# Kernel optimization log

Hardware: AMD Instinct MI355X
Metric: run time of the kernel (lower is better)

Reference implementation:

```python
import jax, jax.numpy as jnp
import numpy as np

B, H, S, D = 2, 16, 2048, 128


def setup_inputs() -> dict:
    key = jax.random.key(0)
    ks = jax.random.split(key, 11)
    s = 1.0 / np.sqrt(D)
    return {
        "query": jax.random.normal(ks[0], (B, H, S, D), dtype=jnp.float32),
        "key": jax.random.normal(ks[1], (B, H, S, D), dtype=jnp.float32),
        "value": jax.random.normal(ks[2], (B, H, S, D), dtype=jnp.float32),
        "Wq": jax.random.normal(ks[3], (D, D), dtype=jnp.float32) * s,
        "bq": jnp.zeros((D,), dtype=jnp.float32),
        "Wk": jax.random.normal(ks[4], (D, D), dtype=jnp.float32) * s,
        "bk": jnp.zeros((D,), dtype=jnp.float32),
        "Wv": jax.random.normal(ks[5], (D, D), dtype=jnp.float32) * s,
        "bv": jnp.zeros((D,), dtype=jnp.float32),
        "Wo": jax.random.normal(ks[6], (D, D), dtype=jnp.float32) * s,
        "bo": jnp.zeros((D,), dtype=jnp.float32),
    }


def reference(query, key, value, Wq, bq, Wk, bk, Wv, bv, Wo, bo):
    # Linear projections (torch Linear: x @ W^T + b) on last dim of [B,H,S,D]
    q = jnp.einsum("bhsd,ed->bhse", query, Wq) + bq
    k = jnp.einsum("bhsd,ed->bhse", key, Wk) + bk
    v = jnp.einsum("bhsd,ed->bhse", value, Wv) + bv
    scale = jnp.sqrt(jnp.asarray(D, dtype=q.dtype))
    q = q / scale
    qk = jnp.einsum("bhse,bhte->bhst", q, k)  # [B,H,S,S] scores
    attn = jax.nn.softmax(qk, axis=-1)
    # dropout_p = 0.0 -> identity
    out = jnp.einsum("bhst,bhtd->bhsd", attn, v)
    out = jnp.einsum("bhsd,ed->bhse", out, Wo) + bo
    return out
```

## Files before the change

### kernel.cpp

```cpp
#include <hip/hip_runtime.h>
#include <hip/hip_bf16.h>
#include <type_traits>
#include <math.h>

typedef __bf16 bf16x8 __attribute__((ext_vector_type(8)));
typedef float floatx4 __attribute__((ext_vector_type(4)));
typedef float floatx16 __attribute__((ext_vector_type(16)));

#define S_LEN 2048
#define D_DIM 128
#define NTOK (2 * 16 * 2048)
#define KVB 64
#define NKV (S_LEN / KVB)

template <typename TIN, typename TOUT>
__device__ __forceinline__ void proj_body4(
    const TIN* __restrict__ x, const float* __restrict__ W,
    const float* __restrict__ b, TOUT* __restrict__ y, float out_scale,
    int chunk0, __bf16 (*Wl)[128]) {
  const int tid = threadIdx.x;
  const int wave = tid >> 6, lane = tid & 63;
  const int g = lane >> 4, lr = lane & 15;

  for (int it = 0; it < 16; ++it) {
    int lin = it * 1024 + tid * 4;
    float4 w4 = *reinterpret_cast<const float4*>(W + lin);
    int r = lin >> 7, c = lin & 127;
    Wl[r][c]     = (__bf16)w4.x;
    Wl[r][c + 1] = (__bf16)w4.y;
    Wl[r][c + 2] = (__bf16)w4.z;
    Wl[r][c + 3] = (__bf16)w4.w;
  }
  __syncthreads();

  float be[8];
#pragma unroll
  for (int nt = 0; nt < 8; ++nt) be[nt] = b[nt * 16 + lr];

  for (int ch = 0; ch < 4; ++ch) {
    const int rbase = (chunk0 + ch) * 64;
    const int arow = rbase + wave * 16 + lr;

    floatx4 acc[8];
#pragma unroll
    for (int i = 0; i < 8; ++i) acc[i] = floatx4{0.f, 0.f, 0.f, 0.f};

#pragma unroll
    for (int kc = 0; kc < 4; ++kc) {
      bf16x8 af;
      const TIN* xp = x + (size_t)arow * D_DIM + kc * 32 + g * 8;
      if constexpr (std::is_same<TIN, float>::value) {
        float4 f0 = *reinterpret_cast<const float4*>(xp);
        float4 f1 = *reinterpret_cast<const float4*>(xp + 4);
        af[0] = (__bf16)f0.x; af[1] = (__bf16)f0.y;
        af[2] = (__bf16)f0.z; af[3] = (__bf16)f0.w;
        af[4] = (__bf16)f1.x; af[5] = (__bf16)f1.y;
        af[6] = (__bf16)f1.z; af[7] = (__bf16)f1.w;
      } else {
        af = *reinterpret_cast<const bf16x8*>(xp);
      }
#pragma unroll
      for (int nt = 0; nt < 8; ++nt) {
        bf16x8 wf = *reinterpret_cast<const bf16x8*>(&Wl[nt * 16 + lr][kc * 32 + g * 8]);
        acc[nt] = __builtin_amdgcn_mfma_f32_16x16x32_bf16(af, wf, acc[nt], 0, 0, 0);
      }
    }

#pragma unroll
    for (int nt = 0; nt < 8; ++nt) {
      int e = nt * 16 + lr;
#pragma unroll
      for (int j = 0; j < 4; ++j) {
        int row = rbase + wave * 16 + g * 4 + j;
        float val = (acc[nt][j] + be[nt]) * out_scale;
        y[(size_t)row * D_DIM + e] = (TOUT)val;
      }
    }
  }
}

__global__ __launch_bounds__(256) void qkv_proj_kernel(
    const float* __restrict__ xq, const float* __restrict__ xk,
    const float* __restrict__ xv, const float* __restrict__ Wq,
    const float* __restrict__ Wk, const float* __restrict__ Wv,
    const float* __restrict__ bq, const float* __restrict__ bk,
    const float* __restrict__ bv, __bf16* yq, __bf16* yk, __bf16* yv,
    float qscale) {
  __shared__ alignas(16) __bf16 Wl[128][128];
  const int which = blockIdx.y;
  const float* x = which == 0 ? xq : which == 1 ? xk : xv;
  const float* W = which == 0 ? Wq : which == 1 ? Wk : Wv;
  const float* b = which == 0 ? bq : which == 1 ? bk : bv;
  __bf16* y = which == 0 ? yq : which == 1 ? yk : yv;
  float sc = which == 0 ? qscale : 1.0f;
  proj_body4<float, __bf16>(x, W, b, y, sc, blockIdx.x * 4, Wl);
}

__global__ __launch_bounds__(256) void o_proj_kernel(
    const __bf16* __restrict__ x, const float* __restrict__ W,
    const float* __restrict__ b, float* __restrict__ y) {
  __shared__ alignas(16) __bf16 Wl[128][128];
  proj_body4<__bf16, float>(x, W, b, y, 1.0f, blockIdx.x * 4, Wl);
}

__device__ __forceinline__ unsigned swz(int row, unsigned byteoff) {
  return byteoff ^ (((unsigned)(row ^ (row >> 3)) & 7u) << 4);
}

__device__ __forceinline__ unsigned pack2(float lo, float hi) {
  union { __bf16 h[2]; unsigned u; } r;
  r.h[0] = (__bf16)lo; r.h[1] = (__bf16)hi;
  return r.u;
}

__global__ __launch_bounds__(256, 2) void attn_fused_kernel(
    const __bf16* __restrict__ q, const __bf16* __restrict__ k,
    const __bf16* __restrict__ v, const float* __restrict__ Wo,
    const float* __restrict__ bo, float* __restrict__ out) {
  __shared__ alignas(16) unsigned char smem[65536];

  const int tid = threadIdx.x;
  const int wave = tid >> 6, lane = tid & 63;
  const int ql = lane & 31;
  const int h = lane >> 5;

  const int bh = blockIdx.x;
  const int qbase = blockIdx.y * 128;
  const __bf16* qp = q + (size_t)bh * S_LEN * D_DIM;
  const __bf16* kp = k + (size_t)bh * S_LEN * D_DIM;
  const __bf16* vp = v + (size_t)bh * S_LEN * D_DIM;

  const int qrow = qbase + wave * 32 + ql;
  bf16x8 qf[8];
#pragma unroll
  for (int kc = 0; kc < 8; ++kc)
    qf[kc] = *reinterpret_cast<const bf16x8*>(
        qp + (size_t)qrow * D_DIM + kc * 16 + h * 8);

  floatx16 ot[4];
#pragma unroll
  for (int d = 0; d < 4; ++d)
#pragma unroll
    for (int r = 0; r < 16; ++r) ot[d][r] = 0.f;
  float m_r = -1e30f, l_r = 0.f;

  const int cc = tid & 15;
  const int pr4 = (tid >> 4) * 4;
  const int ce = cc * 8;

  unsigned Rk[4];
#pragma unroll
  for (int x = 0; x < 4; ++x)
    Rk[x] = (unsigned)(h * 1024) +
            (((unsigned)(ql * 16)) ^ ((unsigned)h << 4) ^ ((unsigned)x << 5));
  const unsigned Rv0 = 32768u + (unsigned)(h * 2048) +
                       (((unsigned)(ql * 16)) ^ (((unsigned)(ql >> 3)) << 4));
  const unsigned Rv1 = Rv0 ^ 64u;
  const unsigned kx = ((unsigned)(cc & 7)) << 4;
  unsigned Wk_[4];
#pragma unroll
  for (int j = 0; j < 4; ++j)
    Wk_[j] = ((unsigned)(cc * 1024 + (pr4 + j) * 16)) ^ kx;
  unsigned Wv_[8];
  {
    unsigned vbase = 32768u + (unsigned)((pr4 >> 3) * 2048 + ce * 16 + (pr4 & 7) * 2);
#pragma unroll
    for (int e = 0; e < 8; ++e)
      Wv_[e] = vbase | (((unsigned)e << 4) ^ kx);
  }

  {
    const __bf16* kr = kp + (size_t)pr4 * D_DIM + ce;
    const __bf16* vr = vp + (size_t)pr4 * D_DIM + ce;
    bf16x8 kR[4];
    union { bf16x8 v8; unsigned short s[8]; } vR[4];
#pragma unroll
    for (int j = 0; j < 4; ++j) {
      kR[j] = *reinterpret_cast<const bf16x8*>(kr + j * D_DIM);
      vR[j].v8 = *reinterpret_cast<const bf16x8*>(vr + j * D_DIM);
    }
#pragma unroll
    for (int j = 0; j < 4; ++j)
      *reinterpret_cast<bf16x8*>(smem + Wk_[j]) = kR[j];
#pragma unroll
    for (int e = 0; e < 8; ++e) {
      uint2 w;
      w.x = (unsigned)vR[0].s[e] | ((unsigned)vR[1].s[e] << 16);
      w.y = (unsigned)vR[2].s[e] | ((unsigned)vR[3].s[e] << 16);
      *reinterpret_cast<uint2*>(smem + Wv_[e]) = w;
    }
  }

  const __bf16* krp = kp + ((size_t)KVB + pr4) * D_DIM + ce;
  const __bf16* vrp = vp + ((size_t)KVB + pr4) * D_DIM + ce;

#pragma unroll 2
  for (int t = 0; t < NKV; ++t) {
    const unsigned cb = (unsigned)(t & 1) * 16384u;
    const bool hn = (t + 1 < NKV);

    __syncthreads();

    bf16x8 kR[4];
    union { bf16x8 v8; unsigned short s[8]; } vR[4];
    if (hn) {
#pragma unroll
      for (int j = 0; j < 4; ++j) {
        kR[j] = *reinterpret_cast<const bf16x8*>(krp + j * D_DIM);
        vR[j].v8 = *reinterpret_cast<const bf16x8*>(vrp + j * D_DIM);
      }
      krp += (size_t)KVB * D_DIM;
      vrp += (size_t)KVB * D_DIM;
    }

    floatx16 st[2];
#pragma unroll
    for (int kvh = 0; kvh < 2; ++kvh)
#pragma unroll
      for (int r = 0; r < 16; ++r) st[kvh][r] = 0.f;
    __builtin_amdgcn_s_setprio(1);
#pragma unroll
    for (int kc = 0; kc < 8; ++kc) {
      bf16x8 kf0 = *reinterpret_cast<const bf16x8*>(
          smem + cb + Rk[kc & 3] + (unsigned)(kc * 2048));
      bf16x8 kf1 = *reinterpret_cast<const bf16x8*>(
          smem + cb + Rk[kc & 3] + (unsigned)(kc * 2048 + 512));
      st[0] = __builtin_amdgcn_mfma_f32_32x32x16_bf16(kf0, qf[kc], st[0], 0, 0, 0);
      st[1] = __builtin_amdgcn_mfma_f32_32x32x16_bf16(kf1, qf[kc], st[1], 0, 0, 0);
    }
    __builtin_amdgcn_s_setprio(0);

    if (hn) {
      const unsigned nb = cb ^ 16384u;
#pragma unroll
      for (int j = 0; j < 4; ++j)
        *reinterpret_cast<bf16x8*>(smem + nb + Wk_[j]) = kR[j];
#pragma unroll
      for (int e = 0; e < 8; ++e) {
        uint2 w;
        w.x = (unsigned)vR[0].s[e] | ((unsigned)vR[1].s[e] << 16);
        w.y = (unsigned)vR[2].s[e] | ((unsigned)vR[3].s[e] << 16);
        *reinterpret_cast<uint2*>(smem + nb + Wv_[e]) = w;
      }
    }

    float t8[8];
#pragma unroll
    for (int i = 0; i < 8; ++i)
      t8[i] = fmaxf(fmaxf(st[0][i], st[0][i + 8]), fmaxf(st[1][i], st[1][i + 8]));
    float pmax = fmaxf(fmaxf(fmaxf(t8[0], t8[4]), fmaxf(t8[1], t8[5])),
                       fmaxf(fmaxf(t8[2], t8[6]), fmaxf(t8[3], t8[7])));
    pmax = fmaxf(pmax, __shfl_xor(pmax, 32));
    if (!__all(pmax - m_r <= 8.0f)) {
      float mnew = fmaxf(m_r, pmax);
      float sc_f = __builtin_amdgcn_exp2f(m_r - mnew);
      m_r = mnew;
      l_r *= sc_f;
#pragma unroll
      for (int d = 0; d < 4; ++d)
#pragma unroll
        for (int r = 0; r < 16; ++r) ot[d][r] *= sc_f;
    }
#pragma unroll
    for (int kvh = 0; kvh < 2; ++kvh)
#pragma unroll
      for (int r = 0; r < 16; ++r)
        st[kvh][r] = __builtin_amdgcn_exp2f(st[kvh][r] - m_r);
    float s8[8];
#pragma unroll
    for (int i = 0; i < 8; ++i)
      s8[i] = (st[0][i] + st[0][i + 8]) + (st[1][i] + st[1][i + 8]);
    float psum = ((s8[0] + s8[4]) + (s8[1] + s8[5])) +
                 ((s8[2] + s8[6]) + (s8[3] + s8[7]));
    psum += __shfl_xor(psum, 32);
    l_r += psum;

#pragma unroll
    for (int ks = 0; ks < 4; ++ks) {
      const int kvh = ks >> 1;
      const int r2a = (2 * ks) & 3;
      const int r2b = r2a + 1;
      unsigned ua0 = pack2(st[kvh][r2a * 4 + 0], st[kvh][r2a * 4 + 1]);
      unsigned ua1 = pack2(st[kvh][r2a * 4 + 2], st[kvh][r2a * 4 + 3]);
      unsigned ub0 = pack2(st[kvh][r2b * 4 + 0], st[kvh][r2b * 4 + 1]);
      unsigned ub1 = pack2(st[kvh][r2b * 4 + 2], st[kvh][r2b * 4 + 3]);
      union { unsigned u[4]; bf16x8 v8; } pw;
#if __has_builtin(__builtin_amdgcn_permlane32_swap)
      {
        auto r0 = __builtin_amdgcn_permlane32_swap(ua0, ub0, false, false);
        auto r1 = __builtin_amdgcn_permlane32_swap(ua1, ub1, false, false);
        pw.u[0] = r0[0];
        pw.u[1] = r1[0];
        pw.u[2] = r0[1];
        pw.u[3] = r1[1];
      }
#else
      {
        unsigned a0x = __shfl_xor(ua0, 32), a1x = __shfl_xor(ua1, 32);
        unsigned b0x = __shfl_xor(ub0, 32), b1x = __shfl_xor(ub1, 32);
        pw.u[0] = h ? b0x : ua0;
        pw.u[1] = h ? b1x : ua1;
        pw.u[2] = h ? ub0 : a0x;
        pw.u[3] = h ? ub1 : a1x;
      }
#endif
      __builtin_amdgcn_s_setprio(1);
#pragma unroll
      for (int db = 0; db < 4; ++db) {
        const unsigned base = (db & 1) ? Rv1 : Rv0;
        bf16x8 vf = *reinterpret_cast<const bf16x8*>(
            smem + cb + base + (unsigned)(ks * 4096 + db * 512));
        ot[db] = __builtin_amdgcn_mfma_f32_32x32x16_bf16(vf, pw.v8, ot[db], 0, 0, 0);
      }
      __builtin_amdgcn_s_setprio(0);
    }
  }

  __syncthreads();

  {
    const float inv_l = 1.0f / l_r;
    const int qloc = wave * 32 + ql;
#pragma unroll
    for (int db = 0; db < 4; ++db)
#pragma unroll
      for (int r = 0; r < 16; ++r) {
        int d = db * 32 + (r & 3) + 8 * (r >> 2) + 4 * h;
        *reinterpret_cast<__bf16*>(smem + swz(qloc, qloc * 256u + d * 2u)) =
            (__bf16)(ot[db][r] * inv_l);
      }
  }
  for (int it = 0; it < 16; ++it) {
    int lin = it * 1024 + tid * 4;
    float4 w4 = *reinterpret_cast<const float4*>(Wo + lin);
    int r = lin >> 7, c = lin & 127;
    unsigned off = 32768u + swz(r, (unsigned)(r * 256 + c * 2));
    __bf16 b4[4] = {(__bf16)w4.x, (__bf16)w4.y, (__bf16)w4.z, (__bf16)w4.w};
    *reinterpret_cast<uint2*>(smem + off) = *reinterpret_cast<uint2*>(b4);
  }
  __syncthreads();

  const int g4 = lane >> 4;
  const int lr = lane & 15;
  float be[8];
#pragma unroll
  for (int nt = 0; nt < 8; ++nt) be[nt] = bo[nt * 16 + lr];

#pragma unroll
  for (int rt = 0; rt < 2; ++rt) {
    const int arow = wave * 32 + rt * 16 + lr;
    floatx4 acc[8];
#pragma unroll
    for (int i = 0; i < 8; ++i) acc[i] = floatx4{0.f, 0.f, 0.f, 0.f};
#pragma unroll
    for (int kc = 0; kc < 4; ++kc) {
      bf16x8 af = *reinterpret_cast<const bf16x8*>(
          smem + swz(arow, (unsigned)(arow * 256 + (kc * 32 + g4 * 8) * 2)));
#pragma unroll
      for (int nt = 0; nt < 8; ++nt) {
        int wrow = nt * 16 + lr;
        bf16x8 wf = *reinterpret_cast<const bf16x8*>(
            smem + 32768u + swz(wrow, (unsigned)(wrow * 256 + (kc * 32 + g4 * 8) * 2)));
        acc[nt] = __builtin_amdgcn_mfma_f32_16x16x32_bf16(af, wf, acc[nt], 0, 0, 0);
      }
    }
#pragma unroll
    for (int nt = 0; nt < 8; ++nt) {
      int e = nt * 16 + lr;
#pragma unroll
      for (int j = 0; j < 4; ++j) {
        int row = qbase + wave * 32 + rt * 16 + g4 * 4 + j;
        out[((size_t)bh * S_LEN + row) * D_DIM + e] = acc[nt][j] + be[nt];
      }
    }
  }
}

__global__ __launch_bounds__(256, 2) void attn_kernel(
    const __bf16* __restrict__ q, const __bf16* __restrict__ k,
    const __bf16* __restrict__ v, __bf16* __restrict__ o) {
  __shared__ alignas(16) unsigned char smem[65536];

  const int tid = threadIdx.x;
  const int wave = tid >> 6, lane = tid & 63;
  const int ql = lane & 31;
  const int h = lane >> 5;

  const int bh = blockIdx.x;
  const int qbase = blockIdx.y * 128;
  const __bf16* qp = q + (size_t)bh * S_LEN * D_DIM;
  const __bf16* kp = k + (size_t)bh * S_LEN * D_DIM;
  const __bf16* vp = v + (size_t)bh * S_LEN * D_DIM;
  __bf16* op = o + (size_t)bh * S_LEN * D_DIM;

  const int qrow = qbase + wave * 32 + ql;
  bf16x8 qf[8];
#pragma unroll
  for (int kc = 0; kc < 8; ++kc)
    qf[kc] = *reinterpret_cast<const bf16x8*>(
        qp + (size_t)qrow * D_DIM + kc * 16 + h * 8);

  floatx16 ot[4];
#pragma unroll
  for (int d = 0; d < 4; ++d)
#pragma unroll
    for (int r = 0; r < 16; ++r) ot[d][r] = 0.f;
  float m_r = -1e30f, l_r = 0.f;

  const int cc = tid & 15;
  const int pr4 = (tid >> 4) * 4;
  const int ce = cc * 8;

  unsigned Rk[4];
#pragma unroll
  for (int x = 0; x < 4; ++x)
    Rk[x] = (unsigned)(h * 1024) +
            (((unsigned)(ql * 16)) ^ ((unsigned)h << 4) ^ ((unsigned)x << 5));
  const unsigned Rv0 = 32768u + (unsigned)(h * 2048) +
                       (((unsigned)(ql * 16)) ^ (((unsigned)(ql >> 3)) << 4));
  const unsigned Rv1 = Rv0 ^ 64u;
  const unsigned kx = ((unsigned)(cc & 7)) << 4;
  unsigned Wk_[4];
#pragma unroll
  for (int j = 0; j < 4; ++j)
    Wk_[j] = ((unsigned)(cc * 1024 + (pr4 + j) * 16)) ^ kx;
  unsigned Wv_[8];
  {
    unsigned vbase = 32768u + (unsigned)((pr4 >> 3) * 2048 + ce * 16 + (pr4 & 7) * 2);
#pragma unroll
    for (int e = 0; e < 8; ++e)
      Wv_[e] = vbase | (((unsigned)e << 4) ^ kx);
  }

  {
    const __bf16* kr = kp + (size_t)pr4 * D_DIM + ce;
    const __bf16* vr = vp + (size_t)pr4 * D_DIM + ce;
    bf16x8 kR[4];
    union { bf16x8 v8; unsigned short s[8]; } vR[4];
#pragma unroll
    for (int j = 0; j < 4; ++j) {
      kR[j] = *reinterpret_cast<const bf16x8*>(kr + j * D_DIM);
      vR[j].v8 = *reinterpret_cast<const bf16x8*>(vr + j * D_DIM);
    }
#pragma unroll
    for (int j = 0; j < 4; ++j)
      *reinterpret_cast<bf16x8*>(smem + Wk_[j]) = kR[j];
#pragma unroll
    for (int e = 0; e < 8; ++e) {
      uint2 w;
      w.x = (unsigned)vR[0].s[e] | ((unsigned)vR[1].s[e] << 16);
      w.y = (unsigned)vR[2].s[e] | ((unsigned)vR[3].s[e] << 16);
      *reinterpret_cast<uint2*>(smem + Wv_[e]) = w;
    }
  }

  const __bf16* krp = kp + ((size_t)KVB + pr4) * D_DIM + ce;
  const __bf16* vrp = vp + ((size_t)KVB + pr4) * D_DIM + ce;

#pragma unroll 2
  for (int t = 0; t < NKV; ++t) {
    const unsigned cb = (unsigned)(t & 1) * 16384u;
    const bool hn = (t + 1 < NKV);

    __syncthreads();

    bf16x8 kR[4];
    union { bf16x8 v8; unsigned short s[8]; } vR[4];
    if (hn) {
#pragma unroll
      for (int j = 0; j < 4; ++j) {
        kR[j] = *reinterpret_cast<const bf16x8*>(krp + j * D_DIM);
        vR[j].v8 = *reinterpret_cast<const bf16x8*>(vrp + j * D_DIM);
      }
      krp += (size_t)KVB * D_DIM;
      vrp += (size_t)KVB * D_DIM;
    }

    floatx16 st[2];
#pragma unroll
    for (int kvh = 0; kvh < 2; ++kvh)
#pragma unroll
      for (int r = 0; r < 16; ++r) st[kvh][r] = 0.f;
    __builtin_amdgcn_s_setprio(1);
#pragma unroll
    for (int kc = 0; kc < 8; ++kc) {
      bf16x8 kf0 = *reinterpret_cast<const bf16x8*>(
          smem + cb + Rk[kc & 3] + (unsigned)(kc * 2048));
      bf16x8 kf1 = *reinterpret_cast<const bf16x8*>(
          smem + cb + Rk[kc & 3] + (unsigned)(kc * 2048 + 512));
      st[0] = __builtin_amdgcn_mfma_f32_32x32x16_bf16(kf0, qf[kc], st[0], 0, 0, 0);
      st[1] = __builtin_amdgcn_mfma_f32_32x32x16_bf16(kf1, qf[kc], st[1], 0, 0, 0);
    }
    __builtin_amdgcn_s_setprio(0);

    if (hn) {
      const unsigned nb = cb ^ 16384u;
#pragma unroll
      for (int j = 0; j < 4; ++j)
        *reinterpret_cast<bf16x8*>(smem + nb + Wk_[j]) = kR[j];
#pragma unroll
      for (int e = 0; e < 8; ++e) {
        uint2 w;
        w.x = (unsigned)vR[0].s[e] | ((unsigned)vR[1].s[e] << 16);
        w.y = (unsigned)vR[2].s[e] | ((unsigned)vR[3].s[e] << 16);
        *reinterpret_cast<uint2*>(smem + nb + Wv_[e]) = w;
      }
    }

    float t8[8];
#pragma unroll
    for (int i = 0; i < 8; ++i)
      t8[i] = fmaxf(fmaxf(st[0][i], st[0][i + 8]), fmaxf(st[1][i], st[1][i + 8]));
    float pmax = fmaxf(fmaxf(fmaxf(t8[0], t8[4]), fmaxf(t8[1], t8[5])),
                       fmaxf(fmaxf(t8[2], t8[6]), fmaxf(t8[3], t8[7])));
    pmax = fmaxf(pmax, __shfl_xor(pmax, 32));
    if (!__all(pmax - m_r <= 8.0f)) {
      float mnew = fmaxf(m_r, pmax);
      float sc_f = __builtin_amdgcn_exp2f(m_r - mnew);
      m_r = mnew;
      l_r *= sc_f;
#pragma unroll
      for (int d = 0; d < 4; ++d)
#pragma unroll
        for (int r = 0; r < 16; ++r) ot[d][r] *= sc_f;
    }
#pragma unroll
    for (int kvh = 0; kvh < 2; ++kvh)
#pragma unroll
      for (int r = 0; r < 16; ++r)
        st[kvh][r] = __builtin_amdgcn_exp2f(st[kvh][r] - m_r);
    float s8[8];
#pragma unroll
    for (int i = 0; i < 8; ++i)
      s8[i] = (st[0][i] + st[0][i + 8]) + (st[1][i] + st[1][i + 8]);
    float psum = ((s8[0] + s8[4]) + (s8[1] + s8[5])) +
                 ((s8[2] + s8[6]) + (s8[3] + s8[7]));
    psum += __shfl_xor(psum, 32);
    l_r += psum;

#pragma unroll
    for (int ks = 0; ks < 4; ++ks) {
      const int kvh = ks >> 1;
      const int r2a = (2 * ks) & 3;
      const int r2b = r2a + 1;
      unsigned ua0 = pack2(st[kvh][r2a * 4 + 0], st[kvh][r2a * 4 + 1]);
      unsigned ua1 = pack2(st[kvh][r2a * 4 + 2], st[kvh][r2a * 4 + 3]);
      unsigned ub0 = pack2(st[kvh][r2b * 4 + 0], st[kvh][r2b * 4 + 1]);
      unsigned ub1 = pack2(st[kvh][r2b * 4 + 2], st[kvh][r2b * 4 + 3]);
      union { unsigned u[4]; bf16x8 v8; } pw;
#if __has_builtin(__builtin_amdgcn_permlane32_swap)
      {
        auto r0 = __builtin_amdgcn_permlane32_swap(ua0, ub0, false, false);
        auto r1 = __builtin_amdgcn_permlane32_swap(ua1, ub1, false, false);
        pw.u[0] = r0[0];
        pw.u[1] = r1[0];
        pw.u[2] = r0[1];
        pw.u[3] = r1[1];
      }
#else
      {
        unsigned a0x = __shfl_xor(ua0, 32), a1x = __shfl_xor(ua1, 32);
        unsigned b0x = __shfl_xor(ub0, 32), b1x = __shfl_xor(ub1, 32);
        pw.u[0] = h ? b0x : ua0;
        pw.u[1] = h ? b1x : ua1;
        pw.u[2] = h ? ub0 : a0x;
        pw.u[3] = h ? ub1 : a1x;
      }
#endif
      __builtin_amdgcn_s_setprio(1);
#pragma unroll
      for (int db = 0; db < 4; ++db) {
        const unsigned base = (db & 1) ? Rv1 : Rv0;
        bf16x8 vf = *reinterpret_cast<const bf16x8*>(
            smem + cb + base + (unsigned)(ks * 4096 + db * 512));
        ot[db] = __builtin_amdgcn_mfma_f32_32x32x16_bf16(vf, pw.v8, ot[db], 0, 0, 0);
      }
      __builtin_amdgcn_s_setprio(0);
    }
  }

  __syncthreads();
  const float inv_l = 1.0f / l_r;
  const int qloc = wave * 32 + ql;
#pragma unroll
  for (int db = 0; db < 4; ++db)
#pragma unroll
    for (int r = 0; r < 16; ++r) {
      int d = db * 32 + (r & 3) + 8 * (r >> 2) + 4 * h;
      *reinterpret_cast<__bf16*>(smem + swz(qloc, qloc * 256u + d * 2u)) =
          (__bf16)(ot[db][r] * inv_l);
    }
  __syncthreads();
#pragma unroll
  for (int it = 0; it < 8; ++it) {
    int r = tid >> 1;
    int c = (tid & 1) * 64 + it * 8;
    bf16x8 val = *reinterpret_cast<const bf16x8*>(smem + swz(r, r * 256u + c * 2u));
    *reinterpret_cast<bf16x8*>(op + (size_t)(qbase + r) * D_DIM + c) = val;
  }
}

extern "C" void kernel_launch(void* const* d_in, const int* in_sizes, int n_in,
                              void* d_out, int out_size, void* d_ws, size_t ws_size,
                              hipStream_t stream) {
  const float* query = (const float*)d_in[0];
  const float* key_  = (const float*)d_in[1];
  const float* value = (const float*)d_in[2];
  const float* Wq = (const float*)d_in[3];
  const float* bq = (const float*)d_in[4];
  const float* Wk = (const float*)d_in[5];
  const float* bk = (const float*)d_in[6];
  const float* Wv = (const float*)d_in[7];
  const float* bv = (const float*)d_in[8];
  const float* Wo = (const float*)d_in[9];
  const float* bo = (const float*)d_in[10];

  const size_t nelem = (size_t)NTOK * D_DIM;
  const float qscale = 0.1275174490036f;
  dim3 blk(256);

  if (ws_size >= 3 * nelem * sizeof(__bf16)) {
    __bf16* vws = (__bf16*)d_ws;
    __bf16* qws = vws + nelem;
    __bf16* kws = qws + nelem;

    qkv_proj_kernel<<<dim3(NTOK / 256, 3), blk, 0, stream>>>(
        query, key_, value, Wq, Wk, Wv, bq, bk, bv, qws, kws, vws, qscale);

    attn_fused_kernel<<<dim3(32, 16), blk, 0, stream>>>(
        qws, kws, vws, Wo, bo, (float*)d_out);
  } else {
    __bf16* vws = (__bf16*)d_ws;
    __bf16* aws = vws + nelem;
    __bf16* qws = (__bf16*)d_out;
    __bf16* kws = qws + nelem;

    qkv_proj_kernel<<<dim3(NTOK / 256, 3), blk, 0, stream>>>(
        query, key_, value, Wq, Wk, Wv, bq, bk, bv, qws, kws, vws, qscale);

    attn_kernel<<<dim3(32, 16), blk, 0, stream>>>(qws, kws, vws, aws);

    o_proj_kernel<<<NTOK / 256, blk, 0, stream>>>(aws, Wo, bo, (float*)d_out);
  }
}
```

Measured before the change: 123.5 us.

## Load K fragments directly from global into registers, bypassing LDS staging

K tiles are no longer staged through shared memory. Each wave now loads its MFMA K fragments straight from global memory into 16 register vectors, prefetching the next tile after the score MFMAs. The shared-memory layout is compacted so only V remains there. This removes LDS writes and reads for K and the associated bank traffic. In exchange, register pressure rises substantially and each wave fetches K separately, multiplying global/L2 reads of K.

```diff
diff --git a/kernel.cpp b/kernel.cpp
--- a/kernel.cpp
+++ b/kernel.cpp
@@ -148,40 +148,34 @@
   const int pr4 = (tid >> 4) * 4;
   const int ce = cc * 8;
 
-  unsigned Rk[4];
-#pragma unroll
-  for (int x = 0; x < 4; ++x)
-    Rk[x] = (unsigned)(h * 1024) +
-            (((unsigned)(ql * 16)) ^ ((unsigned)h << 4) ^ ((unsigned)x << 5));
-  const unsigned Rv0 = 32768u + (unsigned)(h * 2048) +
+  const unsigned Rv0 = (unsigned)(h * 2048) +
                        (((unsigned)(ql * 16)) ^ (((unsigned)(ql >> 3)) << 4));
   const unsigned Rv1 = Rv0 ^ 64u;
   const unsigned kx = ((unsigned)(cc & 7)) << 4;
-  unsigned Wk_[4];
-#pragma unroll
-  for (int j = 0; j < 4; ++j)
-    Wk_[j] = ((unsigned)(cc * 1024 + (pr4 + j) * 16)) ^ kx;
   unsigned Wv_[8];
   {
-    unsigned vbase = 32768u + (unsigned)((pr4 >> 3) * 2048 + ce * 16 + (pr4 & 7) * 2);
+    unsigned vbase = (unsigned)((pr4 >> 3) * 2048 + ce * 16 + (pr4 & 7) * 2);
 #pragma unroll
     for (int e = 0; e < 8; ++e)
       Wv_[e] = vbase | (((unsigned)e << 4) ^ kx);
   }
 
+  const __bf16* kgp = kp + (size_t)(ql * 128 + h * 8);
+  bf16x8 kf[16];
+#pragma unroll
+  for (int kvh = 0; kvh < 2; ++kvh)
+#pragma unroll
+    for (int kc = 0; kc < 8; ++kc)
+      kf[kvh * 8 + kc] =
+          *reinterpret_cast<const bf16x8*>(kgp + kvh * 4096 + kc * 16);
+  kgp += (size_t)KVB * D_DIM;
+
   {
-    const __bf16* kr = kp + (size_t)pr4 * D_DIM + ce;
     const __bf16* vr = vp + (size_t)pr4 * D_DIM + ce;
-    bf16x8 kR[4];
     union { bf16x8 v8; unsigned short s[8]; } vR[4];
 #pragma unroll
-    for (int j = 0; j < 4; ++j) {
-      kR[j] = *reinterpret_cast<const bf16x8*>(kr + j * D_DIM);
+    for (int j = 0; j < 4; ++j)
       vR[j].v8 = *reinterpret_cast<const bf16x8*>(vr + j * D_DIM);
-    }
-#pragma unroll
-    for (int j = 0; j < 4; ++j)
-      *reinterpret_cast<bf16x8*>(smem + Wk_[j]) = kR[j];
 #pragma unroll
     for (int e = 0; e < 8; ++e) {
       uint2 w;
@@ -191,7 +185,6 @@
     }
   }
 
-  const __bf16* krp = kp + ((size_t)KVB + pr4) * D_DIM + ce;
   const __bf16* vrp = vp + ((size_t)KVB + pr4) * D_DIM + ce;
 
 #pragma unroll 2
@@ -201,15 +194,11 @@
 
     __syncthreads();
 
-    bf16x8 kR[4];
     union { bf16x8 v8; unsigned short s[8]; } vR[4];
     if (hn) {
 #pragma unroll
-      for (int j = 0; j < 4; ++j) {
-        kR[j] = *reinterpret_cast<const bf16x8*>(krp + j * D_DIM);
+      for (int j = 0; j < 4; ++j)
         vR[j].v8 = *reinterpret_cast<const bf16x8*>(vrp + j * D_DIM);
-      }
-      krp += (size_t)KVB * D_DIM;
       vrp += (size_t)KVB * D_DIM;
     }
 
@@ -221,20 +210,23 @@
     __builtin_amdgcn_s_setprio(1);
 #pragma unroll
     for (int kc = 0; kc < 8; ++kc) {
-      bf16x8 kf0 = *reinterpret_cast<const bf16x8*>(
-          smem + cb + Rk[kc & 3] + (unsigned)(kc * 2048));
-      bf16x8 kf1 = *reinterpret_cast<const bf16x8*>(
-          smem + cb + Rk[kc & 3] + (unsigned)(kc * 2048 + 512));
-      st[0] = __builtin_amdgcn_mfma_f32_32x32x16_bf16(kf0, qf[kc], st[0], 0, 0, 0);
-      st[1] = __builtin_amdgcn_mfma_f32_32x32x16_bf16(kf1, qf[kc], st[1], 0, 0, 0);
+      st[0] = __builtin_amdgcn_mfma_f32_32x32x16_bf16(kf[kc], qf[kc], st[0], 0, 0, 0);
+      st[1] = __builtin_amdgcn_mfma_f32_32x32x16_bf16(kf[8 + kc], qf[kc], st[1], 0, 0, 0);
     }
     __builtin_amdgcn_s_setprio(0);
+
+    if (hn) {
+#pragma unroll
+      for (int kvh = 0; kvh < 2; ++kvh)
+#pragma unroll
+        for (int kc = 0; kc < 8; ++kc)
+          kf[kvh * 8 + kc] =
+              *reinterpret_cast<const bf16x8*>(kgp + kvh * 4096 + kc * 16);
+      kgp += (size_t)KVB * D_DIM;
+    }
 
     if (hn) {
       const unsigned nb = cb ^ 16384u;
-#pragma unroll
-      for (int j = 0; j < 4; ++j)
-        *reinterpret_cast<bf16x8*>(smem + nb + Wk_[j]) = kR[j];
 #pragma unroll
       for (int e = 0; e < 8; ++e) {
         uint2 w;
```

Measured after the change: 168.3 us. 1.36x slower.
